# Kernel tuning notes

Hardware: AMD Instinct MI355X
Metric: run time of the kernel (lower is better)

The kernel has to match this reference:

```python
import jax, jax.numpy as jnp
import numpy as np
import math

B, S, E, H = 2, 4096, 1024, 16
W = 256  # one-sided attention window (attention_window // 2)


def setup_inputs() -> dict:
    key = jax.random.key(0)
    ks = jax.random.split(key, 7)
    init = lambda k, shp: jax.random.normal(k, shp, jnp.float32) * 0.02
    return {
        "hidden_states": jax.random.normal(ks[0], (B, S, E), jnp.float32),
        "attention_mask": jnp.zeros((B, S), jnp.int32),  # 0 = local attention
        "q_w": init(ks[1], (E, E)), "q_b": jnp.zeros((E,), jnp.float32),
        "k_w": init(ks[2], (E, E)), "k_b": jnp.zeros((E,), jnp.float32),
        "v_w": init(ks[3], (E, E)), "v_b": jnp.zeros((E,), jnp.float32),
    }


def _banded_attention(hidden_states, attention_mask, q_w, q_b, k_w, k_b, v_w, v_b):
    D = E // H          # head dim
    w = W               # one-sided window
    nc = S // w         # number of query chunks of length w
    # Projections (torch Linear: x @ W.T + b); query pre-scaled by sqrt(head_dim)
    q = (hidden_states @ q_w.T + q_b) / math.sqrt(D)
    k = hidden_states @ k_w.T + k_b
    v = hidden_states @ v_w.T + v_b
    heads = lambda x: x.reshape(B, S, H, D).transpose(0, 2, 1, 3)  # [B,H,S,D]
    q, k, v = heads(q), heads(k), heads(v)

    qc = q.reshape(B, H, nc, w, D)                       # [B,H,nc,w,D]
    pad = lambda x: jnp.pad(x, ((0, 0), (0, 0), (w, w), (0, 0)))
    # chunk c of keys/values covers padded positions [c*w, c*w + 3w)
    idx = (jnp.arange(nc) * w)[:, None] + jnp.arange(3 * w)[None, :]  # [nc,3w]
    kc = pad(k)[:, :, idx]                               # [B,H,nc,3w,D]
    vc = pad(v)[:, :, idx]                               # [B,H,nc,3w,D]

    # banded scores: query x in chunk attends padded key y; rel offset = y-w-x
    scores = jnp.einsum('bhcxd,bhcyd->bhcxy', qc, kc)    # [B,H,nc,w,3w]

    # additive mask from attention_mask (!=0 -> -10000 at that key position)
    fm = jnp.where(attention_mask != 0, -10000.0, 0.0)   # [B,S]
    fmc = jnp.pad(fm, ((0, 0), (w, w)))[:, idx]          # [B,nc,3w]
    scores = scores + fmc[:, None, :, None, :]

    # validity: |rel| <= w (the 2w+1 band) and key index j in [0, S)
    x = jnp.arange(w)[:, None]                           # [w,1]
    y = jnp.arange(3 * w)[None, :]                       # [1,3w]
    rel = y - w - x                                      # [w,3w]
    j = (jnp.arange(nc) * w)[:, None, None] + (y - w)[None]  # [nc,1,3w] key idx
    valid = (jnp.abs(rel) <= w)[None] & (j >= 0) & (j < S)   # [nc,w,3w]
    scores = jnp.where(valid[None, None], scores, -jnp.inf)

    probs = jax.nn.softmax(scores.astype(jnp.float32), axis=-1)
    ctx = jnp.einsum('bhcxy,bhcyd->bhcxd', probs, vc)    # [B,H,nc,w,D]
    return ctx.reshape(B, H, S, D).transpose(0, 2, 1, 3).reshape(B, S, E)


def reference(hidden_states, attention_mask, q_w, q_b, k_w, k_b, v_w, v_b):
    return _banded_attention(hidden_states, attention_mask,
                             q_w, q_b, k_w, k_b, v_w, v_b)
```

## Files before the change

### kernel.cpp

```cpp
#include <hip/hip_runtime.h>
#include <math.h>

constexpr int Bn  = 2;
constexpr int Sn  = 4096;
constexpr int En  = 1024;
constexpr int Hn  = 16;
constexpr int Mtot = Bn * Sn;
constexpr int Kp  = 1024;
constexpr int PAD = 72;

typedef __bf16    bf16x8 __attribute__((ext_vector_type(8)));
typedef __bf16    bf16x4 __attribute__((ext_vector_type(4)));
typedef _Float16  f16x8  __attribute__((ext_vector_type(8)));
typedef _Float16  f16x4  __attribute__((ext_vector_type(4)));
typedef float     f32x4  __attribute__((ext_vector_type(4)));

__global__ void __launch_bounds__(256)
cvt_hs_kernel(const float* __restrict__ hs, _Float16* __restrict__ hs16)
{
    int t = blockIdx.x * 256 + threadIdx.x;
    int m = t >> 8;
    int k = (t & 255) << 2;
    float4 x = *(const float4*)&hs[((size_t)m << 10) + k];
    f16x4 h;
    h[0] = (_Float16)x.x; h[1] = (_Float16)x.y;
    h[2] = (_Float16)x.z; h[3] = (_Float16)x.w;
    *(f16x4*)&hs16[((size_t)m << 10) + k] = h;
}

__global__ void __launch_bounds__(256)
cvt_w_kernel(const float* __restrict__ qw, const float* __restrict__ kw,
             const float* __restrict__ vw, _Float16* __restrict__ w16)
{
    int t = blockIdx.x * 256 + threadIdx.x;
    int gn = t >> 8;
    int k  = (t & 255) << 2;
    int p  = gn >> 10, n = gn & 1023;
    const float* src = (p == 0) ? qw : (p == 1) ? kw : vw;
    float4 x = *(const float4*)&src[((size_t)n << 10) + k];
    f16x4 h;
    h[0] = (_Float16)x.x; h[1] = (_Float16)x.y;
    h[2] = (_Float16)x.z; h[3] = (_Float16)x.w;
    *(f16x4*)&w16[((size_t)gn << 10) + k] = h;
}

__device__ inline void load_lds16(const void* g, void* s) {
    __builtin_amdgcn_global_load_lds((const __attribute__((address_space(1))) void*)g,
                                     (__attribute__((address_space(3))) void*)s,
                                     16, 0, 0);
}

__global__ void __launch_bounds__(256)
qkv_mfma_kernel(const _Float16* __restrict__ A2, const _Float16* __restrict__ B2,
                const float* __restrict__ qb, const float* __restrict__ kb,
                const float* __restrict__ vb,
                __bf16* __restrict__ q16, __bf16* __restrict__ k16,
                __bf16* __restrict__ vt16)
{
    __shared__ _Float16 As[128 * 32];
    __shared__ _Float16 Bs[128 * 32];

    const int tid  = threadIdx.x;
    const int m0   = blockIdx.x * 128;
    const int n0   = blockIdx.y * 128;
    const int w    = tid >> 6;
    const int lane = tid & 63;
    const int wm   = w >> 1, wn = w & 1;
    const int mrow = lane & 15, quad = lane >> 4;

    const int stRow = w * 16 + (lane >> 2);
    const int stCol = (lane & 3) * 8;

    f32x4 acc[4][4] = {};

    const _Float16* Abase = A2 + (size_t)(m0 + stRow) * Kp + stCol;
    const _Float16* Bbase = B2 + (size_t)(n0 + stRow) * Kp + stCol;
    _Float16* AsW = &As[w * 512];
    _Float16* BsW = &Bs[w * 512];

    for (int k0 = 0; k0 < Kp; k0 += 32) {
        load_lds16(Abase + k0,            AsW);
        load_lds16(Abase + 64 * Kp + k0,  AsW + 2048);
        load_lds16(Bbase + k0,            BsW);
        load_lds16(Bbase + 64 * Kp + k0,  BsW + 2048);
        __syncthreads();
        f16x8 af[4], bfr[4];
#pragma unroll
        for (int t = 0; t < 4; t++) {
            af[t]  = *(const f16x8*)&As[(wm * 64 + t * 16 + mrow) * 32 + quad * 8];
            bfr[t] = *(const f16x8*)&Bs[(wn * 64 + t * 16 + mrow) * 32 + quad * 8];
        }
#pragma unroll
        for (int ti = 0; ti < 4; ti++)
#pragma unroll
            for (int tj = 0; tj < 4; tj++)
                acc[ti][tj] = __builtin_amdgcn_mfma_f32_16x16x32_f16(
                    af[ti], bfr[tj], acc[ti][tj], 0, 0, 0);
        __syncthreads();
    }

    const int p = n0 >> 10;
    const float* bptr = (p == 0) ? qb : (p == 1) ? kb : vb;
#pragma unroll
    for (int tj = 0; tj < 4; tj++) {
        const int n  = n0 + wn * 64 + tj * 16 + mrow;
        const float bv = bptr[n & 1023];
        const int hh = (n & 1023) >> 6, dd = n & 63;
#pragma unroll
        for (int ti = 0; ti < 4; ti++) {
            const int m  = m0 + wm * 64 + ti * 16 + quad * 4;
            const int bb = m >> 12, ss = m & 4095;
            const size_t bhh = (size_t)(bb * Hn + hh);
            if (p == 0) {
#pragma unroll
                for (int r = 0; r < 4; r++)
                    q16[(bhh * Sn + ss + r) * 64 + dd] =
                        (__bf16)((acc[ti][tj][r] + bv) * 0.125f);
            } else if (p == 1) {
#pragma unroll
                for (int r = 0; r < 4; r++)
                    k16[(bhh * Sn + ss + r) * 64 + dd] =
                        (__bf16)(acc[ti][tj][r] + bv);
            } else {
                bf16x4 pv4;
#pragma unroll
                for (int r = 0; r < 4; r++)
                    pv4[r] = (__bf16)(acc[ti][tj][r] + bv);
                *(bf16x4*)&vt16[(bhh * 64 + dd) * (size_t)Sn + ss] = pv4;
            }
        }
    }
}

__global__ void __launch_bounds__(256, 2)
banded_attn_kernel(const __bf16* __restrict__ q16, const __bf16* __restrict__ k16,
                   const __bf16* __restrict__ vt16, const int* __restrict__ mask,
                   float* __restrict__ out)
{
    __shared__ __bf16 Kt[2][64 * PAD];
    __shared__ __bf16 Vt[2][64 * PAD];
    __shared__ __bf16 Pt[4][64 * PAD];
    __shared__ float  Msh[768];

    const int c = blockIdx.x, h = blockIdx.y, b = blockIdx.z;
    const int bh = b * Hn + h;
    const int i0 = c * 256;
    const int jwin0 = i0 - 256;
    const int tid  = threadIdx.x;
    const int wv   = tid >> 6;
    const int lane = tid & 63;
    const int quad = lane >> 4, mrow = lane & 15;

#pragma unroll
    for (int rep = 0; rep < 3; rep++) {
        int idx = rep * 256 + tid;
        int jg  = jwin0 + idx;
        float mv = 0.f;
        if (jg >= 0 && jg < Sn && mask[b * Sn + jg] != 0) mv = -10000.f;
        Msh[idx] = mv;
    }

    bf16x8 qf[4][2];
    const __bf16* qbase = q16 + (((size_t)bh * Sn + i0 + wv * 64) << 6);
#pragma unroll
    for (int tjq = 0; tjq < 4; tjq++)
#pragma unroll
        for (int kc = 0; kc < 2; kc++)
            qf[tjq][kc] = *(const bf16x8*)(qbase + (16 * tjq + mrow) * 64 + 32 * kc + 8 * quad);

    const int sr = lane >> 3;
    const int sc = lane & 7;
    bf16x8 kreg0, kreg1, vreg0, vreg1;
    auto gload = [&](int st) {
        const int j0 = jwin0 + st * 64;
        const int r0 = wv * 16 + sr;
        const int r1 = wv * 16 + 8 + sr;
        int jk0 = j0 + r0; jk0 = jk0 < 0 ? 0 : (jk0 > Sn - 1 ? Sn - 1 : jk0);
        int jk1 = j0 + r1; jk1 = jk1 < 0 ? 0 : (jk1 > Sn - 1 ? Sn - 1 : jk1);
        kreg0 = *(const bf16x8*)&k16[(((size_t)bh * Sn + jk0) << 6) + sc * 8];
        kreg1 = *(const bf16x8*)&k16[(((size_t)bh * Sn + jk1) << 6) + sc * 8];
        int jv = j0 + sc * 8; jv = jv < 0 ? 0 : (jv > Sn - 8 ? Sn - 8 : jv);
        vreg0 = *(const bf16x8*)&vt16[((size_t)bh * 64 + r0) * Sn + jv];
        vreg1 = *(const bf16x8*)&vt16[((size_t)bh * 64 + r1) * Sn + jv];
    };
    auto swrite = [&](int buf) {
        *(bf16x8*)&Kt[buf][(wv * 16 + sr) * PAD + sc * 8]     = kreg0;
        *(bf16x8*)&Kt[buf][(wv * 16 + 8 + sr) * PAD + sc * 8] = kreg1;
        *(bf16x8*)&Vt[buf][(wv * 16 + sr) * PAD + sc * 8]     = vreg0;
        *(bf16x8*)&Vt[buf][(wv * 16 + 8 + sr) * PAD + sc * 8] = vreg1;
    };

    f32x4 acc_o[4][4] = {};
    float lrun[4] = {0.f, 0.f, 0.f, 0.f};
    __bf16* Pw = &Pt[wv][0];

    gload(0);
    swrite(0);
    __syncthreads();

    for (int st = 0; st < 12; st++) {
        const int buf = st & 1;
        if (st + 1 < 12) gload(st + 1);

        if (st >= wv && st <= wv + 8) {
            const __bf16* KtB = &Kt[buf][0];
            const __bf16* VtB = &Vt[buf][0];
#pragma unroll
            for (int ti = 0; ti < 4; ti++) {
                bf16x8 ak0 = *(const bf16x8*)&KtB[(16 * ti + mrow) * PAD + quad * 8];
                bf16x8 ak1 = *(const bf16x8*)&KtB[(16 * ti + mrow) * PAD + 32 + quad * 8];
                const int y0 = 64 * st + 16 * ti + 4 * quad;
                f32x4 ms4 = *(const f32x4*)&Msh[y0];
#pragma unroll
                for (int tjq = 0; tjq < 4; tjq++) {
                    f32x4 s = {};
                    s = __builtin_amdgcn_mfma_f32_16x16x32_bf16(ak0, qf[tjq][0], s, 0, 0, 0);
                    s = __builtin_amdgcn_mfma_f32_16x16x32_bf16(ak1, qf[tjq][1], s, 0, 0, 0);
                    const int xq = 64 * wv + 16 * tjq + mrow;
                    bf16x4 pk;
                    float psum = 0.f;
#pragma unroll
                    for (int r = 0; r < 4; r++) {
                        const int y = y0 + r;
                        bool ok = ((unsigned)(y - xq) <= 512u) &
                                  ((unsigned)(jwin0 + y) < 4096u);
                        float pv = ok ? __expf(s[r] + ms4[r]) : 0.f;
                        psum += pv;
                        pk[r] = (__bf16)pv;
                    }
                    lrun[tjq] += psum;
                    *(bf16x4*)&Pw[(16 * tjq + mrow) * PAD + 16 * ti + 4 * quad] = pk;
                }
            }
#pragma unroll
            for (int kc2 = 0; kc2 < 2; kc2++) {
                bf16x8 av[4];
#pragma unroll
                for (int dt = 0; dt < 4; dt++)
                    av[dt] = *(const bf16x8*)&VtB[(16 * dt + mrow) * PAD + kc2 * 32 + quad * 8];
#pragma unroll
                for (int tjq = 0; tjq < 4; tjq++) {
                    bf16x8 pf = *(const bf16x8*)&Pw[(16 * tjq + mrow) * PAD + kc2 * 32 + quad * 8];
#pragma unroll
                    for (int dt = 0; dt < 4; dt++)
                        acc_o[dt][tjq] = __builtin_amdgcn_mfma_f32_16x16x32_bf16(
                            av[dt], pf, acc_o[dt][tjq], 0, 0, 0);
                }
            }
        }

        if (st + 1 < 12) {
            swrite((st + 1) & 1);
            __syncthreads();
        }
    }

    float inv[4];
#pragma unroll
    for (int tjq = 0; tjq < 4; tjq++) {
        float l = lrun[tjq];
        l += __shfl_xor(l, 16);
        l += __shfl_xor(l, 32);
        inv[tjq] = 1.0f / l;
    }
#pragma unroll
    for (int dt = 0; dt < 4; dt++)
#pragma unroll
        for (int tjq = 0; tjq < 4; tjq++) {
            f32x4 o = acc_o[dt][tjq];
            o[0] *= inv[tjq]; o[1] *= inv[tjq]; o[2] *= inv[tjq]; o[3] *= inv[tjq];
            float* dst = out + ((size_t)(b * Sn + i0 + wv * 64 + 16 * tjq + mrow)) * En
                             + h * 64 + 16 * dt + 4 * quad;
            *(f32x4*)dst = o;
        }
}

extern "C" void kernel_launch(void* const* d_in, const int* in_sizes, int n_in,
                              void* d_out, int out_size, void* d_ws, size_t ws_size,
                              hipStream_t stream) {
    const float* hs  = (const float*)d_in[0];
    const int*  mask = (const int*)d_in[1];
    const float* qw  = (const float*)d_in[2];
    const float* qb  = (const float*)d_in[3];
    const float* kw  = (const float*)d_in[4];
    const float* kb  = (const float*)d_in[5];
    const float* vw  = (const float*)d_in[6];
    const float* vb  = (const float*)d_in[7];
    float* out = (float*)d_out;

    _Float16* hs16 = (_Float16*)d_ws;
    _Float16* w16  = (_Float16*)((char*)d_ws + (size_t)16777216);
    __bf16*   q16  = (__bf16*)((char*)d_ws + (size_t)23068672);
    __bf16*   k16  = (__bf16*)((char*)d_ws + (size_t)39845888);
    __bf16*   vt16 = (__bf16*)((char*)d_ws + (size_t)56623104);

    cvt_hs_kernel<<<8192, 256, 0, stream>>>(hs, hs16);
    cvt_w_kernel <<<3072, 256, 0, stream>>>(qw, kw, vw, w16);

    dim3 pgrid(Mtot / 128, 3072 / 128);
    qkv_mfma_kernel<<<pgrid, 256, 0, stream>>>(hs16, w16, qb, kb, vb, q16, k16, vt16);

    dim3 agrid(Sn / 256, Hn, Bn);
    banded_attn_kernel<<<agrid, 256, 0, stream>>>(q16, k16, vt16, mask, out);
}
```

Before: 215.7 us.

## Double-buffer QKV GEMM LDS tiles, swizzle LDS layout, vectorize Q/K stores

The QKV projection GEMM now double-buffers its LDS tiles, so the next k-slice's global-to-LDS loads are issued before computing on the current one, and one barrier per iteration is removed. LDS columns are XOR-swizzled on both write and read to cut bank conflicts. For Q and K the MFMA operands are swapped so each lane holds four consecutive output features, which allows 8-byte vectorized bf16 stores and float4 bias loads instead of scattered 2-byte stores. The cost is double the LDS footprint, which may lower occupancy, and extra branching on the projection type.

```diff
diff --git a/kernel.cpp b/kernel.cpp
--- a/kernel.cpp
+++ b/kernel.cpp
@@ -57,8 +57,8 @@
                 __bf16* __restrict__ q16, __bf16* __restrict__ k16,
                 __bf16* __restrict__ vt16)
 {
-    __shared__ _Float16 As[128 * 32];
-    __shared__ _Float16 Bs[128 * 32];
+    __shared__ _Float16 As[2][128 * 32];
+    __shared__ _Float16 Bs[2][128 * 32];
 
     const int tid  = threadIdx.x;
     const int m0   = blockIdx.x * 128;
@@ -67,66 +67,96 @@
     const int lane = tid & 63;
     const int wm   = w >> 1, wn = w & 1;
     const int mrow = lane & 15, quad = lane >> 4;
+    const int p    = n0 >> 10;
 
     const int stRow = w * 16 + (lane >> 2);
-    const int stCol = (lane & 3) * 8;
+    const int stCol = (((lane & 3) ^ ((lane >> 3) & 3))) * 8;
+
+    const int rq = ((quad ^ ((mrow >> 1) & 3))) * 8;
 
     f32x4 acc[4][4] = {};
 
     const _Float16* Abase = A2 + (size_t)(m0 + stRow) * Kp + stCol;
     const _Float16* Bbase = B2 + (size_t)(n0 + stRow) * Kp + stCol;
-    _Float16* AsW = &As[w * 512];
-    _Float16* BsW = &Bs[w * 512];
-
-    for (int k0 = 0; k0 < Kp; k0 += 32) {
+
+    auto stage = [&](int k0, int buf) {
+        _Float16* AsW = &As[buf][w * 512];
+        _Float16* BsW = &Bs[buf][w * 512];
         load_lds16(Abase + k0,            AsW);
         load_lds16(Abase + 64 * Kp + k0,  AsW + 2048);
         load_lds16(Bbase + k0,            BsW);
         load_lds16(Bbase + 64 * Kp + k0,  BsW + 2048);
+    };
+
+    stage(0, 0);
+    __syncthreads();
+
+    for (int k0 = 0; k0 < Kp; k0 += 32) {
+        const int cur = (k0 >> 5) & 1;
+        if (k0 + 32 < Kp) stage(k0 + 32, cur ^ 1);
+
+        f16x8 af[4], bfr[4];
+        const _Float16* AsR = &As[cur][0];
+        const _Float16* BsR = &Bs[cur][0];
+#pragma unroll
+        for (int t = 0; t < 4; t++) {
+            af[t]  = *(const f16x8*)&AsR[(wm * 64 + t * 16 + mrow) * 32 + rq];
+            bfr[t] = *(const f16x8*)&BsR[(wn * 64 + t * 16 + mrow) * 32 + rq];
+        }
+        if (p < 2) {
+#pragma unroll
+            for (int ti = 0; ti < 4; ti++)
+#pragma unroll
+                for (int tj = 0; tj < 4; tj++)
+                    acc[ti][tj] = __builtin_amdgcn_mfma_f32_16x16x32_f16(
+                        bfr[tj], af[ti], acc[ti][tj], 0, 0, 0);
+        } else {
+#pragma unroll
+            for (int ti = 0; ti < 4; ti++)
+#pragma unroll
+                for (int tj = 0; tj < 4; tj++)
+                    acc[ti][tj] = __builtin_amdgcn_mfma_f32_16x16x32_f16(
+                        af[ti], bfr[tj], acc[ti][tj], 0, 0, 0);
+        }
         __syncthreads();
-        f16x8 af[4], bfr[4];
-#pragma unroll
-        for (int t = 0; t < 4; t++) {
-            af[t]  = *(const f16x8*)&As[(wm * 64 + t * 16 + mrow) * 32 + quad * 8];
-            bfr[t] = *(const f16x8*)&Bs[(wn * 64 + t * 16 + mrow) * 32 + quad * 8];
-        }
-#pragma unroll
-        for (int ti = 0; ti < 4; ti++)
-#pragma unroll
-            for (int tj = 0; tj < 4; tj++)
-                acc[ti][tj] = __builtin_amdgcn_mfma_f32_16x16x32_f16(
-                    af[ti], bfr[tj], acc[ti][tj], 0, 0, 0);
-        __syncthreads();
-    }
-
-    const int p = n0 >> 10;
-    const float* bptr = (p == 0) ? qb : (p == 1) ? kb : vb;
-#pragma unroll
-    for (int tj = 0; tj < 4; tj++) {
-        const int n  = n0 + wn * 64 + tj * 16 + mrow;
-        const float bv = bptr[n & 1023];
-        const int hh = (n & 1023) >> 6, dd = n & 63;
+    }
+
+    if (p < 2) {
+        const float* bptr = (p == 0) ? qb : kb;
+        __bf16* dst = (p == 0) ? q16 : k16;
+        const float scl = (p == 0) ? 0.125f : 1.0f;
 #pragma unroll
         for (int ti = 0; ti < 4; ti++) {
-            const int m  = m0 + wm * 64 + ti * 16 + quad * 4;
+            const int m  = m0 + wm * 64 + ti * 16 + mrow;
             const int bb = m >> 12, ss = m & 4095;
-            const size_t bhh = (size_t)(bb * Hn + hh);
-            if (p == 0) {
-#pragma unroll
-                for (int r = 0; r < 4; r++)
-                    q16[(bhh * Sn + ss + r) * 64 + dd] =
-                        (__bf16)((acc[ti][tj][r] + bv) * 0.125f);
-            } else if (p == 1) {
-#pragma unroll
-                for (int r = 0; r < 4; r++)
-                    k16[(bhh * Sn + ss + r) * 64 + dd] =
-                        (__bf16)(acc[ti][tj][r] + bv);
-            } else {
+#pragma unroll
+            for (int tj = 0; tj < 4; tj++) {
+                const int fl = (n0 + wn * 64 + tj * 16 + quad * 4) & 1023;
+                const int hh = fl >> 6, dd = fl & 63;
+                const float4 bv = *(const float4*)&bptr[fl];
+                bf16x4 o;
+                o[0] = (__bf16)((acc[ti][tj][0] + bv.x) * scl);
+                o[1] = (__bf16)((acc[ti][tj][1] + bv.y) * scl);
+                o[2] = (__bf16)((acc[ti][tj][2] + bv.z) * scl);
+                o[3] = (__bf16)((acc[ti][tj][3] + bv.w) * scl);
+                *(bf16x4*)&dst[((size_t)(bb * Hn + hh) * Sn + ss) * 64 + dd] = o;
+            }
+        }
+    } else {
+#pragma unroll
+        for (int tj = 0; tj < 4; tj++) {
+            const int n  = n0 + wn * 64 + tj * 16 + mrow;
+            const float bv = vb[n & 1023];
+            const int hh = (n & 1023) >> 6, dd = n & 63;
+#pragma unroll
+            for (int ti = 0; ti < 4; ti++) {
+                const int m  = m0 + wm * 64 + ti * 16 + quad * 4;
+                const int bb = m >> 12, ss = m & 4095;
                 bf16x4 pv4;
 #pragma unroll
                 for (int r = 0; r < 4; r++)
                     pv4[r] = (__bf16)(acc[ti][tj][r] + bv);
-                *(bf16x4*)&vt16[(bhh * 64 + dd) * (size_t)Sn + ss] = pv4;
+                *(bf16x4*)&vt16[((size_t)(bb * Hn + hh) * 64 + dd) * Sn + ss] = pv4;
             }
         }
     }
```

Measured after the change: 234.4 us. 1.09x slower.
